# Performance work log

Hardware: AMD Instinct MI355X
Metric: run time of the kernel (lower is better)

Reference implementation:

```python
import jax, jax.numpy as jnp
from jax import lax
import numpy as np


def _lstm_layer(x, W_ih, W_hh, b_ih, b_hh):
    # x: (T, B, in_dim); gate order i, f, g, o (PyTorch convention)
    T, B, _ = x.shape
    H = W_hh.shape[1]
    # precompute input projections for all timesteps (one big GEMM)
    x_proj = jnp.einsum('tbi,gi->tbg', x, W_ih) + b_ih + b_hh  # (T, B, 4H)

    def step(carry, xt):
        h, c = carry
        gates = xt + h @ W_hh.T  # (B, 4H)
        i, f, g, o = jnp.split(gates, 4, axis=-1)
        c = jax.nn.sigmoid(f) * c + jax.nn.sigmoid(i) * jnp.tanh(g)
        h = jax.nn.sigmoid(o) * jnp.tanh(c)
        return (h, c), h

    h0 = jnp.zeros((B, H), dtype=x.dtype)
    c0 = jnp.zeros((B, H), dtype=x.dtype)
    (hT, cT), hs = lax.scan(step, (h0, c0), x_proj)
    return hs, hT, cT


def setup_inputs() -> dict:
    key = jax.random.key(0)
    ks = jax.random.split(key, 12)
    T, B, D_in, H, D_out = 1024, 64, 256, 512, 256
    s_in = 1.0 / np.sqrt(H)
    inp = {
        'x': jax.random.normal(ks[0], (T, B, D_in), jnp.float32),
        'W_ih0': jax.random.uniform(ks[1], (4 * H, D_in), jnp.float32, -s_in, s_in),
        'W_hh0': jax.random.uniform(ks[2], (4 * H, H), jnp.float32, -s_in, s_in),
        'b_ih0': jax.random.uniform(ks[3], (4 * H,), jnp.float32, -s_in, s_in),
        'b_hh0': jax.random.uniform(ks[4], (4 * H,), jnp.float32, -s_in, s_in),
        'W_ih1': jax.random.uniform(ks[5], (4 * H, H), jnp.float32, -s_in, s_in),
        'W_hh1': jax.random.uniform(ks[6], (4 * H, H), jnp.float32, -s_in, s_in),
        'b_ih1': jax.random.uniform(ks[7], (4 * H,), jnp.float32, -s_in, s_in),
        'b_hh1': jax.random.uniform(ks[8], (4 * H,), jnp.float32, -s_in, s_in),
        'W_out': jax.random.uniform(ks[9], (D_out, H), jnp.float32, -s_in, s_in),
        'b_out': jax.random.uniform(ks[10], (D_out,), jnp.float32, -s_in, s_in),
    }
    return inp


def reference(x, W_ih0, W_hh0, b_ih0, b_hh0, W_ih1, W_hh1, b_ih1, b_hh1, W_out, b_out):
    h1s, h1, c1 = _lstm_layer(x, W_ih0, W_hh0, b_ih0, b_hh0)
    h2s, h2, c2 = _lstm_layer(h1s, W_ih1, W_hh1, b_ih1, b_hh1)
    out = jnp.einsum('tbh,oh->tbo', h2s, W_out) + b_out  # (T, B, D_out)
    hn = jnp.stack([h1, h2], axis=0)  # (num_layers, B, H)
    cn = jnp.stack([c1, c2], axis=0)
    return (out, hn, cn)
```

## Files before the change

### kernel.cpp

```cpp
#include <hip/hip_runtime.h>

#define TT   1024
#define BB   64
#define DIN  256
#define HH   512
#define DOUT 256

#define NWG_L0  64
#define NWG_L1  128
#define NWG_OUT 8
#define NWG_TOT 200

typedef short bf16x8 __attribute__((ext_vector_type(8)));
typedef float f32x4  __attribute__((ext_vector_type(4)));
typedef unsigned u32x4 __attribute__((ext_vector_type(4)));

__device__ bf16x8 g_xf[TT * 2048];
__device__ bf16x8 g_h1f[4][4096];
__device__ bf16x8 g_h2f[4][4096];
__device__ bf16x8 g_h1z[4096];
__device__ bf16x8 g_h2z[4096];

__device__ unsigned g_sync[4 * 4 * 4 * 16];
__device__ unsigned g_iter;

__device__ __forceinline__ unsigned* syncp(int kind, int ct, int slot) {
    return &g_sync[(((kind * 4) + ct) * 4 + slot) * 16];
}

__device__ __forceinline__ u32x4 ldg_cv16(const void* p) {
    u32x4 r;
    asm volatile("global_load_dwordx4 %0, %1, off sc0 sc1"
                 : "=&v"(r) : "v"(p) : "memory");
    return r;
}
__device__ __forceinline__ void stg_cv_u16(void* p, unsigned v) {
    asm volatile("global_store_short %0, %1, off sc0 sc1" :: "v"(p), "v"(v) : "memory");
}
__device__ __forceinline__ void wait_vm0(void) {
    asm volatile("s_waitcnt vmcnt(0)" ::: "memory");
}

__device__ __forceinline__ void waitpoll(const unsigned* p, unsigned tgt, int active, int tid) {
    if (tid < 64) {
        for (;;) {
            unsigned v = 0xFFFFFFFFu;
            if (active)
                asm volatile("global_load_dword %0, %1, off sc0 sc1\n\t"
                             "s_waitcnt vmcnt(0)"
                             : "=&v"(v) : "v"(p) : "memory");
            if (__all(v >= tgt)) break;
            __builtin_amdgcn_s_sleep(1);
        }
    }
    __syncthreads();
}

__device__ __forceinline__ float sigf(float v) { return 1.f / (1.f + __expf(-v)); }
__device__ __forceinline__ float tanh_fast(float v) { return 2.f / (1.f + __expf(-2.f * v)) - 1.f; }

__device__ __forceinline__ short f2bf(float f) {
    unsigned u = __builtin_bit_cast(unsigned, f);
    unsigned r = (u + 0x7FFFu + ((u >> 16) & 1u)) >> 16;
    return (short)r;
}

__device__ __forceinline__ bf16x8 pack8(float4 v0, float4 v1) {
    bf16x8 r;
    r[0] = f2bf(v0.x); r[1] = f2bf(v0.y); r[2] = f2bf(v0.z); r[3] = f2bf(v0.w);
    r[4] = f2bf(v1.x); r[5] = f2bf(v1.y); r[6] = f2bf(v1.z); r[7] = f2bf(v1.w);
    return r;
}

extern "C" __global__ void __launch_bounds__(256)
pack_x(const float* __restrict__ x) {
    const int t = blockIdx.x, tid = threadIdx.x;
    const float* xt = x + (size_t)t * BB * DIN;
    bf16x8* dst = g_xf + (size_t)t * 2048;
    #pragma unroll
    for (int u = 0; u < 8; ++u) {
        const int f = u * 256 + tid;
        const int lane_ = f & 63, ctks = f >> 6;
        const int ct = ctks & 3, ks = ctks >> 2;
        const int b  = ct * 16 + (lane_ & 15);
        const int kb = ks * 32 + (lane_ >> 4) * 8;
        const float4* s = (const float4*)(xt + b * DIN + kb);
        dst[f] = pack8(s[0], s[1]);
    }
}

template<int L, int NCT>
__device__ void run_layer(int lwg, int tid,
                          const float* __restrict__ wih, const float* __restrict__ whh,
                          const float* __restrict__ bih, const float* __restrict__ bhh,
                          float* __restrict__ out, unsigned Q, bf16x8* sB)
{
    constexpr int KINX = (L == 0) ? DIN : HH;
    constexpr int NKSA = KINX / 32;
    constexpr int NKS  = NKSA + HH / 32;
    constexpr int ROWS = NKS * NCT;
    constexpr int NST  = ROWS / 4;
    constexpr int NCXR = (L == 0) ? (NKSA * NCT / 4) : 0;

    const int lane = tid & 63, lo = lane & 15, hi = lane >> 4;
    const int w      = tid >> 6;
    const int ctbase = (NCT == 2) ? (lwg & 1) * 2 : (lwg & 3);
    const int ub     = (NCT == 2) ? (lwg >> 1) : (lwg >> 2);
    const int wv     = ub * 4 + w;
    const int jbase  = wv * 4;
    const int grow   = (lo & 3) * HH + jbase + (lo >> 2);

    bf16x8 aF[NKS];
    #pragma unroll
    for (int ks = 0; ks < NKS; ++ks) {
        const float* wr;
        if (ks < NKSA) wr = wih + (size_t)grow * KINX + ks * 32 + hi * 8;
        else           wr = whh + (size_t)grow * HH + (ks - NKSA) * 32 + hi * 8;
        const float4* p = (const float4*)wr;
        aF[ks] = pack8(p[0], p[1]);
    }

    f32x4 biasv;
    #pragma unroll
    for (int r = 0; r < 4; ++r)
        biasv[r] = bih[r * HH + jbase + hi] + bhh[r * HH + jbase + hi];

    const int wksp = wv >> 3, wkhi = (wv >> 1) & 3, wel = (wv & 1) * 4 + hi;

    const unsigned cpb = Q * 8192u;
    float cst[NCT];
    #pragma unroll
    for (int c = 0; c < NCT; ++c) cst[c] = 0.f;

    for (int t = 0; t < TT; ++t) {
        const unsigned* wp = syncp(0, 0, 0); unsigned wt = 0; int wa = 0;
        if (L == 0) {
            if (lane < 2) {
                if (t > 0) { wp = syncp(0, ctbase + lane, (t - 1) & 3);
                             wt = cpb + 32u * (((t - 1) >> 2) + 1); wa = 1; }
            } else if (lane < 4) {
                if (t >= 4) { wp = syncp(2, ctbase + lane - 2, t & 3);
                              wt = Q * 16384u + 64u * (((t - 4) >> 2) + 1); wa = 1; }
            }
        } else {
            if (lane == 0) { wp = syncp(0, ctbase, t & 3);
                             wt = cpb + 32u * ((t >> 2) + 1); wa = 1; }
            else if (lane == 1) { if (t > 0) { wp = syncp(1, ctbase, (t - 1) & 3);
                                               wt = cpb + 32u * (((t - 1) >> 2) + 1); wa = 1; } }
            else if (lane == 2) { if (t >= 4) { wp = syncp(3, ctbase, t & 3);
                                                wt = Q * 9216u + 36u * (((t - 4) >> 2) + 1); wa = 1; } }
        }
        waitpoll(wp, wt, wa, tid);

        const bf16x8* srcA = (L == 0) ? (g_xf + (size_t)t * 2048) : g_h1f[t & 3];
        const bf16x8* srcB = (L == 0) ? ((t == 0) ? g_h1z : g_h1f[(t - 1) & 3])
                                      : ((t == 0) ? g_h2z : g_h2f[(t - 1) & 3]);

        u32x4 stg[NST];
        #pragma unroll
        for (int r = 0; r < NST; ++r) {
            const int ri = r * 4 + w;
            const int ks = ri / NCT, c = ri % NCT;
            if (r < NCXR) {
                stg[r] = *(const u32x4*)&srcA[(ks * 4 + ctbase + c) * 64 + lane];
            } else {
                const bf16x8* src = (ks < NKSA)
                    ? &srcA[(ks * 4 + ctbase + c) * 64 + lane]
                    : &srcB[((ks - NKSA) * 4 + ctbase + c) * 64 + lane];
                stg[r] = ldg_cv16(src);
            }
        }
        wait_vm0();
        #pragma unroll
        for (int r = 0; r < NST; ++r)
            ((u32x4*)sB)[(r * 4 + w) * 64 + lane] = stg[r];
        __syncthreads();

        if (L == 0) {
            if (t > 0 && tid < 2) atomicAdd(syncp(2, ctbase + tid, (t - 1) & 3), 1u);
        } else {
            if (tid == 0) atomicAdd(syncp(2, ctbase, t & 3), 1u);
            if (tid == 1 && t > 0) atomicAdd(syncp(3, ctbase, (t - 1) & 3), 1u);
        }

        f32x4 acc[NCT];
        #pragma unroll
        for (int c = 0; c < NCT; ++c) acc[c] = biasv;
        #pragma unroll
        for (int ks = 0; ks < NKS; ++ks)
            #pragma unroll
            for (int c = 0; c < NCT; ++c)
                acc[c] = __builtin_amdgcn_mfma_f32_16x16x32_bf16(
                    aF[ks], sB[(ks * NCT + c) * 64 + lane], acc[c], 0, 0, 0);

        short* ringW = (short*)((L == 0) ? g_h1f[t & 3] : g_h2f[t & 3]);
        #pragma unroll
        for (int c = 0; c < NCT; ++c) {
            const int ct = ctbase + c;
            const float gi = acc[c][0], gf = acc[c][1];
            const float gg = acc[c][2], go = acc[c][3];
            const float cn_ = sigf(gf) * cst[c] + sigf(gi) * tanh_fast(gg);
            const float hv  = sigf(go) * tanh_fast(cn_);
            cst[c] = cn_;
            stg_cv_u16(&ringW[(((wksp * 4 + ct) * 64) + wkhi * 16 + lo) * 8 + wel],
                       (unsigned)(unsigned short)f2bf(hv));
            if (t == TT - 1) {
                const int j = jbase + hi, b = ct * 16 + lo;
                const size_t base = (size_t)TT * BB * DOUT;
                out[base + (size_t)L * BB * HH + (size_t)b * HH + j] = hv;
                out[base + (size_t)2 * BB * HH + (size_t)L * BB * HH + (size_t)b * HH + j] = cn_;
            }
        }
        wait_vm0();
        __syncthreads();
        if (L == 0) { if (tid < 2) atomicAdd(syncp(0, ctbase + tid, t & 3), 1u); }
        else        { if (tid == 0) atomicAdd(syncp(1, ctbase, t & 3), 1u); }
    }
    if (L == 0) { if (tid < 2) atomicAdd(syncp(2, ctbase + tid, 3), 1u); }
    else        { if (tid == 0) atomicAdd(syncp(3, ctbase, 3), 1u); }
}

__device__ void run_out(int lwg, int tid,
                        const float* __restrict__ wout, const float* __restrict__ bout,
                        float* __restrict__ out, unsigned Q, bf16x8* sB)
{
    constexpr int NKS  = HH / 32;
    constexpr int NST  = 8;
    const int lane = tid & 63, lo = lane & 15, hi = lane >> 4;
    const int w = tid >> 6;
    const int ctbase = (lwg & 1) * 2, ob = lwg >> 1;
    const int obase = (ob * 4 + w) * 16;
    const unsigned cpb = Q * 8192u;

    bf16x8 aF[NKS];
    #pragma unroll
    for (int ks = 0; ks < NKS; ++ks) {
        const float4* p = (const float4*)(wout + (size_t)(obase + lo) * HH + ks * 32 + hi * 8);
        aF[ks] = pack8(p[0], p[1]);
    }
    f32x4 biasv;
    #pragma unroll
    for (int r = 0; r < 4; ++r) biasv[r] = bout[obase + hi * 4 + r];

    for (int t = 0; t < TT; ++t) {
        const unsigned* wp = syncp(0, 0, 0); unsigned wt = 0; int wa = 0;
        if (lane < 2) { wp = syncp(1, ctbase + lane, t & 3);
                        wt = cpb + 32u * ((t >> 2) + 1); wa = 1; }
        waitpoll(wp, wt, wa, tid);

        const bf16x8* src = g_h2f[t & 3];
        u32x4 stg[NST];
        #pragma unroll
        for (int r = 0; r < NST; ++r) {
            const int ri = r * 4 + w;
            const int ks = ri >> 1, c = ri & 1;
            stg[r] = ldg_cv16(&src[(ks * 4 + ctbase + c) * 64 + lane]);
        }
        wait_vm0();
        #pragma unroll
        for (int r = 0; r < NST; ++r)
            ((u32x4*)sB)[(r * 4 + w) * 64 + lane] = stg[r];
        __syncthreads();
        if (tid < 2) atomicAdd(syncp(3, ctbase + tid, t & 3), 1u);

        f32x4 acc[2] = {biasv, biasv};
        #pragma unroll
        for (int ks = 0; ks < NKS; ++ks)
            #pragma unroll
            for (int c = 0; c < 2; ++c)
                acc[c] = __builtin_amdgcn_mfma_f32_16x16x32_bf16(
                    aF[ks], sB[(ks * 2 + c) * 64 + lane], acc[c], 0, 0, 0);
        #pragma unroll
        for (int c = 0; c < 2; ++c)
            #pragma unroll
            for (int r = 0; r < 4; ++r) {
                const int b = (ctbase + c) * 16 + lo, o = obase + hi * 4 + r;
                out[(size_t)t * BB * DOUT + (size_t)b * DOUT + o] = acc[c][r];
            }
    }
}

extern "C" __global__ void __launch_bounds__(256, 1)
lstm2_fused(const float* __restrict__ x,
            const float* __restrict__ wih0, const float* __restrict__ whh0,
            const float* __restrict__ bih0, const float* __restrict__ bhh0,
            const float* __restrict__ wih1, const float* __restrict__ whh1,
            const float* __restrict__ bih1, const float* __restrict__ bhh1,
            const float* __restrict__ wout, const float* __restrict__ bout,
            float* __restrict__ out)
{
    __shared__ bf16x8 sB[3072];

    const int tid = threadIdx.x, wg = blockIdx.x;
    const unsigned Q = __hip_atomic_load(&g_iter, __ATOMIC_RELAXED, __HIP_MEMORY_SCOPE_AGENT);

    if (wg < NWG_L0)
        run_layer<0, 2>(wg, tid, wih0, whh0, bih0, bhh0, out, Q, sB);
    else if (wg < NWG_L0 + NWG_L1)
        run_layer<1, 1>(wg - NWG_L0, tid, wih1, whh1, bih1, bhh1, out, Q, sB);
    else
        run_out(wg - NWG_L0 - NWG_L1, tid, wout, bout, out, Q, sB);

    if (wg == 0 && tid == 0)
        __hip_atomic_store(&g_iter, Q + 1, __ATOMIC_RELAXED, __HIP_MEMORY_SCOPE_AGENT);
}

extern "C" void kernel_launch(void* const* d_in, const int* in_sizes, int n_in,
                              void* d_out, int out_size, void* d_ws, size_t ws_size,
                              hipStream_t stream) {
    const float* x    = (const float*)d_in[0];
    const float* wih0 = (const float*)d_in[1];
    const float* whh0 = (const float*)d_in[2];
    const float* bih0 = (const float*)d_in[3];
    const float* bhh0 = (const float*)d_in[4];
    const float* wih1 = (const float*)d_in[5];
    const float* whh1 = (const float*)d_in[6];
    const float* bih1 = (const float*)d_in[7];
    const float* bhh1 = (const float*)d_in[8];
    const float* wout = (const float*)d_in[9];
    const float* bout = (const float*)d_in[10];
    float* out = (float*)d_out;

    hipLaunchKernelGGL(pack_x, dim3(TT), dim3(256), 0, stream, x);
    hipLaunchKernelGGL(lstm2_fused, dim3(NWG_TOT), dim3(256), 0, stream,
                       x, wih0, whh0, bih0, bhh0, wih1, whh1, bih1, bhh1,
                       wout, bout, out);
}
```

Before: 4.483 ms.

## Replace atomic counter barriers with per-workgroup epoch flag stores

Each workgroup now writes its own flag with a plain coherent store of a monotonic epoch value, replacing the shared atomic counters across workgroups. Waiters poll many flags in parallel across lanes and waves. The aim is to remove contention on hot atomic counters and the read-modify-write latency on the per-timestep critical path. In exchange, every wait polls more memory locations, and correctness relies on epoch values from prior launches (Q-based offsets) staying ordered.

Result: faster. 3.858 ms (-14.0%).

```diff
diff --git a/kernel.cpp b/kernel.cpp
--- a/kernel.cpp
+++ b/kernel.cpp
@@ -21,12 +21,10 @@
 __device__ bf16x8 g_h1z[4096];
 __device__ bf16x8 g_h2z[4096];
 
-__device__ unsigned g_sync[4 * 4 * 4 * 16];
+__device__ unsigned g_flg[520 * 16];
 __device__ unsigned g_iter;
 
-__device__ __forceinline__ unsigned* syncp(int kind, int ct, int slot) {
-    return &g_sync[(((kind * 4) + ct) * 4 + slot) * 16];
-}
+__device__ __forceinline__ unsigned* FLG(int idx) { return &g_flg[idx * 16]; }
 
 __device__ __forceinline__ u32x4 ldg_cv16(const void* p) {
     u32x4 r;
@@ -37,21 +35,22 @@
 __device__ __forceinline__ void stg_cv_u16(void* p, unsigned v) {
     asm volatile("global_store_short %0, %1, off sc0 sc1" :: "v"(p), "v"(v) : "memory");
 }
+__device__ __forceinline__ void stg_cv_u32(void* p, unsigned v) {
+    asm volatile("global_store_dword %0, %1, off sc0 sc1" :: "v"(p), "v"(v) : "memory");
+}
 __device__ __forceinline__ void wait_vm0(void) {
     asm volatile("s_waitcnt vmcnt(0)" ::: "memory");
 }
 
 __device__ __forceinline__ void waitpoll(const unsigned* p, unsigned tgt, int active, int tid) {
-    if (tid < 64) {
-        for (;;) {
-            unsigned v = 0xFFFFFFFFu;
-            if (active)
-                asm volatile("global_load_dword %0, %1, off sc0 sc1\n\t"
-                             "s_waitcnt vmcnt(0)"
-                             : "=&v"(v) : "v"(p) : "memory");
-            if (__all(v >= tgt)) break;
-            __builtin_amdgcn_s_sleep(1);
-        }
+    for (;;) {
+        unsigned v = 0xFFFFFFFFu;
+        if (active)
+            asm volatile("global_load_dword %0, %1, off sc0 sc1\n\t"
+                         "s_waitcnt vmcnt(0)"
+                         : "=&v"(v) : "v"(p) : "memory");
+        if (__all(v >= tgt)) break;
+        __builtin_amdgcn_s_sleep(1);
     }
     __syncthreads();
 }
@@ -105,6 +104,7 @@
     const int lane = tid & 63, lo = lane & 15, hi = lane >> 4;
     const int w      = tid >> 6;
     const int ctbase = (NCT == 2) ? (lwg & 1) * 2 : (lwg & 3);
+    const int grp    = (NCT == 2) ? (lwg & 1) : (lwg & 3);
     const int ub     = (NCT == 2) ? (lwg >> 1) : (lwg >> 2);
     const int wv     = ub * 4 + w;
     const int jbase  = wv * 4;
@@ -127,28 +127,35 @@
 
     const int wksp = wv >> 3, wkhi = (wv >> 1) & 3, wel = (wv & 1) * 4 + hi;
 
-    const unsigned cpb = Q * 8192u;
+    const unsigned Qb = Q * 2048u;
     float cst[NCT];
     #pragma unroll
     for (int c = 0; c < NCT; ++c) cst[c] = 0.f;
 
     for (int t = 0; t < TT; ++t) {
-        const unsigned* wp = syncp(0, 0, 0); unsigned wt = 0; int wa = 0;
+        const unsigned* wp = g_flg; unsigned wt = 0; int wa = 0;
         if (L == 0) {
-            if (lane < 2) {
-                if (t > 0) { wp = syncp(0, ctbase + lane, (t - 1) & 3);
-                             wt = cpb + 32u * (((t - 1) >> 2) + 1); wa = 1; }
-            } else if (lane < 4) {
-                if (t >= 4) { wp = syncp(2, ctbase + lane - 2, t & 3);
-                              wt = Q * 16384u + 64u * (((t - 4) >> 2) + 1); wa = 1; }
+            if (w == 0) {
+                if (lane < 32 && t >= 1) { wp = FLG(0 + grp * 32 + lane); wt = Qb + t; wa = 1; }
+            } else if (w == 1) {
+                if (t >= 4) { wp = FLG(192 + (grp * 2 + (lane >> 5)) * 32 + (lane & 31));
+                              wt = Qb + t - 3; wa = 1; }
+            } else if (w == 2) {
+                if (lane < 32 && t >= 4) { wp = FLG(320 + grp * 32 + lane);
+                                           wt = Qb + t - 3; wa = 1; }
             }
         } else {
-            if (lane == 0) { wp = syncp(0, ctbase, t & 3);
-                             wt = cpb + 32u * ((t >> 2) + 1); wa = 1; }
-            else if (lane == 1) { if (t > 0) { wp = syncp(1, ctbase, (t - 1) & 3);
-                                               wt = cpb + 32u * (((t - 1) >> 2) + 1); wa = 1; } }
-            else if (lane == 2) { if (t >= 4) { wp = syncp(3, ctbase, t & 3);
-                                                wt = Q * 9216u + 36u * (((t - 4) >> 2) + 1); wa = 1; } }
+            if (w == 0) {
+                if (lane < 32) {
+                    wp = FLG(0 + (grp >> 1) * 32 + lane); wt = Qb + t + 1; wa = 1;
+                } else if (t >= 1) {
+                    wp = FLG(64 + grp * 32 + (lane - 32)); wt = Qb + t; wa = 1;
+                }
+            } else if (w == 1 && t >= 4) {
+                if (lane < 32)      { wp = FLG(384 + grp * 32 + lane); wt = Qb + t - 3; wa = 1; }
+                else if (lane < 36) { wp = FLG(512 + (grp >> 1) * 4 + (lane - 32));
+                                      wt = Qb + t - 3; wa = 1; }
+            }
         }
         waitpoll(wp, wt, wa, tid);
 
@@ -177,10 +184,10 @@
         __syncthreads();
 
         if (L == 0) {
-            if (t > 0 && tid < 2) atomicAdd(syncp(2, ctbase + tid, (t - 1) & 3), 1u);
+            if (tid == 0) stg_cv_u32(FLG(320 + grp * 32 + ub), Qb + t);
         } else {
-            if (tid == 0) atomicAdd(syncp(2, ctbase, t & 3), 1u);
-            if (tid == 1 && t > 0) atomicAdd(syncp(3, ctbase, (t - 1) & 3), 1u);
+            if (tid == 0) stg_cv_u32(FLG(192 + grp * 32 + ub), Qb + t + 1);
+            if (tid == 1) stg_cv_u32(FLG(384 + grp * 32 + ub), Qb + t);
         }
 
         f32x4 acc[NCT];
@@ -213,11 +220,9 @@
         }
         wait_vm0();
         __syncthreads();
-        if (L == 0) { if (tid < 2) atomicAdd(syncp(0, ctbase + tid, t & 3), 1u); }
-        else        { if (tid == 0) atomicAdd(syncp(1, ctbase, t & 3), 1u); }
-    }
-    if (L == 0) { if (tid < 2) atomicAdd(syncp(2, ctbase + tid, 3), 1u); }
-    else        { if (tid == 0) atomicAdd(syncp(3, ctbase, 3), 1u); }
+        if (L == 0) { if (tid == 0) stg_cv_u32(FLG(0 + grp * 32 + ub), Qb + t + 1); }
+        else        { if (tid == 0) stg_cv_u32(FLG(64 + grp * 32 + ub), Qb + t + 1); }
+    }
 }
 
 __device__ void run_out(int lwg, int tid,
@@ -228,9 +233,10 @@
     constexpr int NST  = 8;
     const int lane = tid & 63, lo = lane & 15, hi = lane >> 4;
     const int w = tid >> 6;
-    const int ctbase = (lwg & 1) * 2, ob = lwg >> 1;
+    const int cp = lwg & 1, ob = lwg >> 1;
+    const int ctbase = cp * 2;
     const int obase = (ob * 4 + w) * 16;
-    const unsigned cpb = Q * 8192u;
+    const unsigned Qb = Q * 2048u;
 
     bf16x8 aF[NKS];
     #pragma unroll
@@ -243,9 +249,11 @@
     for (int r = 0; r < 4; ++r) biasv[r] = bout[obase + hi * 4 + r];
 
     for (int t = 0; t < TT; ++t) {
-        const unsigned* wp = syncp(0, 0, 0); unsigned wt = 0; int wa = 0;
-        if (lane < 2) { wp = syncp(1, ctbase + lane, t & 3);
-                        wt = cpb + 32u * ((t >> 2) + 1); wa = 1; }
+        const unsigned* wp = g_flg; unsigned wt = 0; int wa = 0;
+        if (w == 0) {
+            wp = FLG(64 + (ctbase + (lane >> 5)) * 32 + (lane & 31));
+            wt = Qb + t + 1; wa = 1;
+        }
         waitpoll(wp, wt, wa, tid);
 
         const bf16x8* src = g_h2f[t & 3];
@@ -261,7 +269,7 @@
         for (int r = 0; r < NST; ++r)
             ((u32x4*)sB)[(r * 4 + w) * 64 + lane] = stg[r];
         __syncthreads();
-        if (tid < 2) atomicAdd(syncp(3, ctbase + tid, t & 3), 1u);
+        if (tid == 0) stg_cv_u32(FLG(512 + cp * 4 + ob), Qb + t + 1);
 
         f32x4 acc[2] = {biasv, biasv};
         #pragma unroll
```
